# Kernel tuning notes

Hardware: AMD Instinct MI355X
Metric: run time of the kernel (lower is better)

The kernel has to match this reference:

```python
import jax, jax.numpy as jnp
import numpy as np

H, KV, D, S = 32, 8, 128, 2048
HID = H * D
L = S  # cache length
LAYER_IDX = 0


def rotate_half(x, axis):
    x1, x2 = jnp.split(x, 2, axis=axis)
    return jnp.concatenate([-x2, x1], axis=axis)


def setup_inputs() -> dict:
    key = jax.random.key(0)
    ks = jax.random.split(key, 9)
    scale = 0.02
    hidden_states = jax.random.normal(ks[0], (1, HID, 1, S), jnp.float32)
    wq = jax.random.normal(ks[1], (H * D, HID), jnp.float32) * scale
    wk = jax.random.normal(ks[2], (KV * D, HID), jnp.float32) * scale
    wv = jax.random.normal(ks[3], (KV * D, HID), jnp.float32) * scale
    wo = jax.random.normal(ks[4], (HID, H * D), jnp.float32) * scale
    bq = jax.random.normal(ks[5], (H * D,), jnp.float32) * scale
    bk = jax.random.normal(ks[6], (KV * D,), jnp.float32) * scale
    bv = jax.random.normal(ks[7], (KV * D,), jnp.float32) * scale
    # RoPE tables (rotate-half convention): (1,1,S,D) and transposed (1,1,D,S)
    inv_freq = 1.0 / (10000.0 ** (np.arange(0, D, 2, dtype=np.float32) / D))
    t = np.arange(S, dtype=np.float32)
    freqs = np.outer(t, inv_freq)                    # (S, D/2)
    emb = np.concatenate([freqs, freqs], axis=-1)    # (S, D)
    cos = jnp.asarray(np.cos(emb), jnp.float32)[None, None]
    sin = jnp.asarray(np.sin(emb), jnp.float32)[None, None]
    cos_t = jnp.swapaxes(cos, -1, -2)
    sin_t = jnp.swapaxes(sin, -1, -2)
    # causal mask in transposed (cache_len, q_len) layout: key pos l visible iff l <= s
    lpos = np.arange(L)[:, None]
    spos = np.arange(S)[None, :]
    attention_mask = jnp.asarray(np.where(lpos <= spos, 0.0, -1e9).astype(np.float32))[None, None]
    key_cache = jnp.zeros((1, KV, L, D), jnp.float32)
    value_cache = jnp.zeros((1, KV, L, D), jnp.float32)
    return dict(hidden_states=hidden_states, wq=wq, bq=bq, wk=wk, bk=bk, wv=wv, bv=bv,
                wo=wo, cos=cos, sin=sin, cos_t=cos_t, sin_t=sin_t,
                attention_mask=attention_mask, key_cache=key_cache,
                value_cache=value_cache, cache_position=0)


def reference(hidden_states, wq, bq, wk, bk, wv, bv, wo, cos, sin, cos_t, sin_t,
              attention_mask, key_cache, value_cache, cache_position):
    x = hidden_states[0, :, 0, :]                          # (HID, S) channels-first
    q = wq @ x + bq[:, None]                               # (H*D, S)
    k = wk @ x + bk[:, None]                               # (KV*D, S)
    v = wv @ x + bv[:, None]
    q = q.reshape(H, D, S)                                 # (H, D, S)
    k = jnp.swapaxes(k.reshape(KV, D, S), 1, 2)            # (KV, S, D)
    v = jnp.swapaxes(v.reshape(KV, D, S), 1, 2)            # (KV, S, D)
    # RoPE: Q rotated along D (dim=-2 in NCHW), K along last dim
    q = q * cos_t[0] + rotate_half(q, axis=1) * sin_t[0]
    k = k * cos[0] + rotate_half(k, axis=2) * sin[0]
    # KV-cache in-place update at cache_position
    kc = jax.lax.dynamic_update_slice(key_cache, k[None], (LAYER_IDX, 0, cache_position, 0))
    vc = jax.lax.dynamic_update_slice(value_cache, v[None], (LAYER_IDX, 0, cache_position, 0))
    kk = kc[LAYER_IDX]                                     # (KV, L, D)
    vv = vc[LAYER_IDX]                                     # (KV, L, D)
    G = H // KV
    qg = q.reshape(KV, G, D, S)                            # group queries per KV head
    scores = jnp.einsum('kld,kgds->kgls', kk, qg) / jnp.sqrt(jnp.float32(D))
    scores = scores + attention_mask[0]                    # (1,L,S) broadcasts over (KV,G,L,S)
    w = jax.nn.softmax(scores, axis=2)                     # softmax over cache_len
    out = jnp.einsum('kgls,kld->kgsd', w, vv)              # (KV, G, S, D)
    out = jnp.swapaxes(out.reshape(H, S, D), 1, 2).reshape(H * D, S)
    y = wo @ out                                           # (HID, S)
    return y[None, :, None, :]                             # (1, HID, 1, S)
```

## Files before the change

### kernel.cpp

```cpp
#include <hip/hip_runtime.h>
#include <hip/hip_bf16.h>

#define H_   32
#define KV_  8
#define D_   128
#define S_   2048
#define HID_ 4096

typedef __attribute__((ext_vector_type(8))) short short8;
typedef short8 short8a __attribute__((may_alias));
typedef __attribute__((ext_vector_type(4))) float f32x4;
typedef unsigned short u16;
typedef unsigned int u32;

__device__ __forceinline__ u16 f2bf(float f) {
  union { float f; unsigned u; } a; a.f = f;
  unsigned r = a.u + 0x7fffu + ((a.u >> 16) & 1u);
  return (u16)(r >> 16);
}
__device__ __forceinline__ float bf2f(u16 h) {
  union { unsigned u; float f; } a; a.u = ((unsigned)h) << 16;
  return a.f;
}

#define GLOAD16(g, l) __builtin_amdgcn_global_load_lds( \
    (const __attribute__((address_space(1))) void*)(g), \
    (__attribute__((address_space(3))) void*)(l), 16, 0, 0)

__global__ void cast4_kernel(const float* __restrict__ s0, const float* __restrict__ s1,
                             const float* __restrict__ s2, const float* __restrict__ s3,
                             u16* __restrict__ d0, u16* __restrict__ d1,
                             u16* __restrict__ d2, u16* __restrict__ d3,
                             int n0, int n1, int n2, int n3) {
  int total = n0 + n1 + n2 + n3;
  for (int i = blockIdx.x * blockDim.x + threadIdx.x; i < total; i += gridDim.x * blockDim.x) {
    const float* s; u16* d; int k = i;
    if (k < n0) { s = s0; d = d0; }
    else if ((k -= n0) < n1) { s = s1; d = d1; }
    else if ((k -= n1) < n2) { s = s2; d = d2; }
    else { k -= n2; s = s3; d = d3; }
    float4 v = ((const float4*)s)[k];
    ushort4 o;
    o.x = f2bf(v.x); o.y = f2bf(v.y); o.z = f2bf(v.z); o.w = f2bf(v.w);
    ((ushort4*)d)[k] = o;
  }
}

__global__ __launch_bounds__(256) void transpose_cast_kernel(const float* __restrict__ in,
                                                             u16* __restrict__ out) {
  __shared__ float t[32][33];
  int tx = threadIdx.x & 31, ty = threadIdx.x >> 5;
  int s0 = blockIdx.x * 32, c0 = blockIdx.y * 32;
  #pragma unroll
  for (int i = 0; i < 4; i++)
    t[ty + i * 8][tx] = in[(size_t)(c0 + ty + i * 8) * S_ + s0 + tx];
  __syncthreads();
  #pragma unroll
  for (int i = 0; i < 4; i++)
    out[(size_t)(s0 + ty + i * 8) * HID_ + c0 + tx] = f2bf(t[tx][ty + i * 8]);
}

__device__ __forceinline__ short8 ldsfrag(const u16* base, int row, int ks, int kg) {
  int cb = (ks * 64 + kg * 16) ^ ((row & 7) << 4);
  return *(const short8a*)((const char*)base + row * 128 + cb);
}

template<int BM>
__global__ __launch_bounds__(512, 2) void gemm_t(const u16* __restrict__ A, const u16* __restrict__ Bt,
    const float* __restrict__ bq, const float* __restrict__ bk, const float* __restrict__ bv,
    u16* __restrict__ Cb, float* __restrict__ Cf, int N, int K) {
  constexpr int CA = BM / 64;
  constexpr int MI = BM / 64;
  __shared__ alignas(16) u16 Asl[2][BM * 64];
  __shared__ alignas(16) u16 Bsl[2][256 * 64];
  int tid = threadIdx.x, wid = tid >> 6, lane = tid & 63;
  int lr = lane & 15, kg = lane >> 4;
  int gx = gridDim.x, nwg = gx * gridDim.y;
  int lid = blockIdx.y * gx + blockIdx.x;
  int q = nwg >> 3, r = nwg & 7;
  int xcd = lid & 7, idx = lid >> 3;
  int swz = (xcd < r ? xcd * (q + 1) : r * (q + 1) + (xcd - r) * q) + idx;
  int m0 = (swz / gx) * BM, n0 = (swz % gx) * 256;
  const u16* Ap = A + (size_t)m0 * K;
  const u16* Bp = Bt + (size_t)n0 * K;
  int wm = wid >> 2, wn = wid & 3;
  f32x4 acc[2][2][MI][2] = {};
  int NT = K >> 6;

  auto STAGEC = [&](const u16* gp, int tile, int chunk, u16* base) {
    int p = tid * 16;
    int row = (chunk << 6) + (p >> 7);
    int gcb = (p & 127) ^ ((row & 7) << 4);
    const char* src = (const char*)gp + ((size_t)row * K + (tile << 6)) * 2 + gcb;
    char* dst = (char*)base + (chunk << 13) + (wid << 10);
    GLOAD16(src, dst);
  };
  auto LDA = [&](short8 (&af)[MI][2], const u16* base, int qm) {
    #pragma unroll
    for (int mi = 0; mi < MI; mi++)
      #pragma unroll
      for (int ks = 0; ks < 2; ks++)
        af[mi][ks] = ldsfrag(base, wm * (BM / 2) + qm * (BM / 4) + mi * 16 + lr, ks, kg);
  };
  auto LDB = [&](short8 (&bf)[2][2], const u16* base, int qn) {
    #pragma unroll
    for (int ni = 0; ni < 2; ni++)
      #pragma unroll
      for (int ks = 0; ks < 2; ks++)
        bf[ni][ks] = ldsfrag(base, wn * 64 + qn * 32 + ni * 16 + lr, ks, kg);
  };
  auto MM = [&](f32x4 (&a)[MI][2], short8 (&af)[MI][2], short8 (&bf)[2][2]) {
    #pragma unroll
    for (int ks = 0; ks < 2; ks++)
      #pragma unroll
      for (int mi = 0; mi < MI; mi++)
        #pragma unroll
        for (int ni = 0; ni < 2; ni++)
          a[mi][ni] = __builtin_amdgcn_mfma_f32_16x16x32_bf16(af[mi][ks], bf[ni][ks], a[mi][ni], 0, 0, 0);
  };
  #define BAR() __builtin_amdgcn_s_barrier()
  #define SB()  __builtin_amdgcn_sched_barrier(0)
  #define VMCNT(n) asm volatile("s_waitcnt vmcnt(" #n ")" ::: "memory")

  #pragma unroll
  for (int c = 0; c < CA; c++) STAGEC(Ap, 0, c, &Asl[0][0]);
  #pragma unroll
  for (int c = 0; c < 4; c++) STAGEC(Bp, 0, c, &Bsl[0][0]);
  #pragma unroll
  for (int c = 0; c < 4; c++) STAGEC(Bp, 1, c, &Bsl[1][0]);
  VMCNT(4);
  BAR();

  short8 af0[MI][2], af1[MI][2], bfA[2][2], bfB[2][2];
  for (int T = 0; T < NT; T++) {
    int par = T & 1;
    u16* aC = &Asl[par][0];
    u16* bC = &Bsl[par][0];
    u16* aN = &Asl[par ^ 1][0];
    int tA = T + 1 < NT ? T + 1 : NT - 1;
    int tB = T + 2 < NT ? T + 2 : NT - 1;
    LDA(af0, aC, 0); LDA(af1, aC, 1); LDB(bfA, bC, 0); LDB(bfB, bC, 1);
    #pragma unroll
    for (int c = 0; c < CA; c++) STAGEC(Ap, tA, c, aN);
    SB(); BAR();
    __builtin_amdgcn_s_setprio(1);
    MM(acc[0][0], af0, bfA); MM(acc[0][1], af0, bfB);
    __builtin_amdgcn_s_setprio(0);
    BAR();
    STAGEC(Bp, tB, 0, bC); STAGEC(Bp, tB, 1, bC);
    STAGEC(Bp, tB, 2, bC); STAGEC(Bp, tB, 3, bC);
    VMCNT(4);
    SB(); BAR();
    __builtin_amdgcn_s_setprio(1);
    MM(acc[1][0], af1, bfA); MM(acc[1][1], af1, bfB);
    __builtin_amdgcn_s_setprio(0);
    BAR();
  }
  #undef BAR
  #undef SB
  #undef VMCNT

  #pragma unroll
  for (int qm = 0; qm < 2; qm++)
    #pragma unroll
    for (int qn = 0; qn < 2; qn++)
      #pragma unroll
      for (int mi = 0; mi < MI; mi++)
        #pragma unroll
        for (int ni = 0; ni < 2; ni++) {
          int col = n0 + wn * 64 + qn * 32 + ni * 16 + lr;
          int rbase = m0 + wm * (BM / 2) + qm * (BM / 4) + mi * 16 + kg * 4;
          #pragma unroll
          for (int rr = 0; rr < 4; rr++) {
            int row = rbase + rr;
            float v = acc[qm][qn][mi][ni][rr];
            if (bq) v += row < 4096 ? bq[row] : (row < 5120 ? bk[row - 4096] : bv[row - 5120]);
            if (Cf) Cf[(size_t)row * N + col] = v;
            else    Cb[(size_t)row * N + col] = f2bf(v);
          }
        }
}

__global__ __launch_bounds__(256, 2) void gemm128(const u16* __restrict__ A, const u16* __restrict__ Bt,
                                                  float* __restrict__ Cf, int N, int K) {
  __shared__ alignas(16) u16 Asl[2][128 * 64];
  __shared__ alignas(16) u16 Bsl[2][128 * 64];
  int tid = threadIdx.x, wid = tid >> 6, lane = tid & 63;
  int lr = lane & 15, kg = lane >> 4;
  int gx = gridDim.x, nwg = gx * gridDim.y;
  int lid = blockIdx.y * gx + blockIdx.x;
  int q = nwg >> 3, r = nwg & 7;
  int xcd = lid & 7, idx = lid >> 3;
  int swz = (xcd < r ? xcd * (q + 1) : r * (q + 1) + (xcd - r) * q) + idx;
  int m0 = (swz / gx) * 128, n0 = (swz % gx) * 128;
  const u16* Ap = A + (size_t)m0 * K;
  const u16* Bp = Bt + (size_t)n0 * K;
  int wr = wid >> 1, wc = wid & 1;
  f32x4 acc[2][2][2][2] = {};
  int NT = K >> 6;

  auto STAGEC = [&](const u16* gp, int tile, int chunk, u16* base) {
    int p = (chunk << 12) + tid * 16;
    int row = p >> 7;
    int gcb = (p & 127) ^ ((row & 7) << 4);
    const char* src = (const char*)gp + ((size_t)row * K + (tile << 6)) * 2 + gcb;
    char* dst = (char*)base + (chunk << 12) + (wid << 10);
    GLOAD16(src, dst);
  };
  auto LDA = [&](short8 (&af)[2][2], const u16* base, int qm) {
    #pragma unroll
    for (int mi = 0; mi < 2; mi++)
      #pragma unroll
      for (int ks = 0; ks < 2; ks++)
        af[mi][ks] = ldsfrag(base, wr * 64 + qm * 32 + mi * 16 + lr, ks, kg);
  };
  auto LDB = [&](short8 (&bf)[2][2], const u16* base, int qn) {
    #pragma unroll
    for (int ni = 0; ni < 2; ni++)
      #pragma unroll
      for (int ks = 0; ks < 2; ks++)
        bf[ni][ks] = ldsfrag(base, wc * 64 + qn * 32 + ni * 16 + lr, ks, kg);
  };
  auto MM = [&](f32x4 (&a)[2][2], short8 (&af)[2][2], short8 (&bf)[2][2]) {
    #pragma unroll
    for (int ks = 0; ks < 2; ks++)
      #pragma unroll
      for (int mi = 0; mi < 2; mi++)
        #pragma unroll
        for (int ni = 0; ni < 2; ni++)
          a[mi][ni] = __builtin_amdgcn_mfma_f32_16x16x32_bf16(af[mi][ks], bf[ni][ks], a[mi][ni], 0, 0, 0);
  };
  #define BAR() __builtin_amdgcn_s_barrier()
  #define SB()  __builtin_amdgcn_sched_barrier(0)
  #define VMCNT(n) asm volatile("s_waitcnt vmcnt(" #n ")" ::: "memory")

  #pragma unroll
  for (int c = 0; c < 4; c++) STAGEC(Ap, 0, c, &Asl[0][0]);
  #pragma unroll
  for (int c = 0; c < 4; c++) STAGEC(Bp, 0, c, &Bsl[0][0]);
  #pragma unroll
  for (int c = 0; c < 4; c++) STAGEC(Bp, 1, c, &Bsl[1][0]);
  VMCNT(4);
  BAR();

  short8 af0[2][2], af1[2][2], bfA[2][2], bfB[2][2];
  for (int T = 0; T < NT; T++) {
    int par = T & 1;
    u16* aC = &Asl[par][0];
    u16* bC = &Bsl[par][0];
    u16* aN = &Asl[par ^ 1][0];
    int tA = T + 1 < NT ? T + 1 : NT - 1;
    int tB = T + 2 < NT ? T + 2 : NT - 1;
    LDA(af0, aC, 0); LDA(af1, aC, 1); LDB(bfA, bC, 0); LDB(bfB, bC, 1);
    STAGEC(Ap, tA, 0, aN); STAGEC(Ap, tA, 1, aN);
    STAGEC(Ap, tA, 2, aN); STAGEC(Ap, tA, 3, aN);
    SB(); BAR();
    __builtin_amdgcn_s_setprio(1);
    MM(acc[0][0], af0, bfA); MM(acc[0][1], af0, bfB);
    __builtin_amdgcn_s_setprio(0);
    BAR();
    STAGEC(Bp, tB, 0, bC); STAGEC(Bp, tB, 1, bC);
    STAGEC(Bp, tB, 2, bC); STAGEC(Bp, tB, 3, bC);
    VMCNT(4);
    SB(); BAR();
    __builtin_amdgcn_s_setprio(1);
    MM(acc[1][0], af1, bfA); MM(acc[1][1], af1, bfB);
    __builtin_amdgcn_s_setprio(0);
    BAR();
  }
  #undef BAR
  #undef SB
  #undef VMCNT

  #pragma unroll
  for (int qm = 0; qm < 2; qm++)
    #pragma unroll
    for (int qn = 0; qn < 2; qn++)
      #pragma unroll
      for (int mi = 0; mi < 2; mi++)
        #pragma unroll
        for (int ni = 0; ni < 2; ni++) {
          int col = n0 + wc * 64 + qn * 32 + ni * 16 + lr;
          int rbase = m0 + wr * 64 + qm * 32 + mi * 16 + kg * 4;
          #pragma unroll
          for (int rr = 0; rr < 4; rr++)
            Cf[(size_t)(rbase + rr) * N + col] = acc[qm][qn][mi][ni][rr];
        }
}

__global__ __launch_bounds__(256) void rope2_kernel(const u16* __restrict__ qin,
                                                    const u16* __restrict__ kin,
                                                    u16* __restrict__ qout,
                                                    u16* __restrict__ kout,
                                                    const float* __restrict__ cp,
                                                    const float* __restrict__ sp) {
  __shared__ u16 t[128][33];
  int hh = blockIdx.x;
  bool isQ = hh < H_;
  int h = isQ ? hh : hh - H_;
  const u16* in = (isQ ? qin : kin) + (size_t)h * 128 * S_;
  u16* out = (isQ ? qout : kout) + (size_t)h * S_ * D_;
  float oscale = isQ ? 0.1275176329533421f : 1.0f;
  int s0 = blockIdx.y * 32;
  int tid = threadIdx.x;
  #pragma unroll
  for (int i = 0; i < 16; i++) {
    int idx = tid + i * 256;
    int row = idx >> 5, sc = idx & 31;
    t[row][sc] = in[(size_t)row * S_ + s0 + sc];
  }
  __syncthreads();
  int d = tid & 127, sh = tid >> 7;
  int dl = d & 63;
  bool hi = d >= 64;
  #pragma unroll
  for (int j = 0; j < 16; j++) {
    int sl = sh * 16 + j;
    int s = s0 + sl;
    float x = bf2f(t[d][sl]);
    float p = bf2f(t[d ^ 64][sl]);
    float c  = cp[(size_t)s * D_ + dl];
    float sn = sp[(size_t)s * D_ + dl];
    float o = hi ? fmaf(p, sn, x * c) : fmaf(-p, sn, x * c);
    out[(size_t)s * D_ + d] = f2bf(o * oscale);
  }
}

__global__ __launch_bounds__(256) void attn_v2(const u16* __restrict__ Q, const u16* __restrict__ K,
                                               const u16* __restrict__ V, u16* __restrict__ Ot) {
  __shared__ alignas(16) u16 Ks[2][64 * 128];
  __shared__ alignas(16) u16 Vs[2][128 * 64];
  __shared__ alignas(16) u16 Pl[4][2][16 * 64];
  int h = blockIdx.x;
  int qtile = (int)(gridDim.y - 1) - (int)blockIdx.y;
  int kv = h >> 2;
  int tid = threadIdx.x, wid = tid >> 6, lane = tid & 63;
  int lr = lane & 15, kg = lane >> 4;
  int q0w = qtile * 128 + wid * 32;
  const u16* Qb = Q + ((size_t)h * S_ + q0w) * D_;
  const u16* Kb = K + (size_t)kv * S_ * D_;
  const u16* Vb = V + (size_t)kv * D_ * S_;
  int sw = (lr & 7) << 3;

  short8 qf[2][4];
  #pragma unroll
  for (int m = 0; m < 2; m++)
    #pragma unroll
    for (int kk = 0; kk < 4; kk++)
      qf[m][kk] = *(const short8a*)(Qb + (size_t)(m * 16 + lr) * D_ + kk * 32 + kg * 8);

  f32x4 acc[2][8] = {};
  float mreg[2] = {-1e30f, -1e30f};
  float lsum[2] = {0.f, 0.f};

  int krow[4], kcb[4], vrow[4], vcb[4];
  #pragma unroll
  for (int j = 0; j < 4; j++) {
    int c = wid * 4 + j;
    int o = c * 1024 + lane * 16;
    krow[j] = o >> 8;
    kcb[j] = (o & 255) ^ ((krow[j] & 7) << 4);
    vrow[j] = o >> 7;
    vcb[j] = (o & 127) ^ ((vrow[j] & 7) << 4);
  }

  int nlt = 2 * qtile + 2;
  #pragma unroll
  for (int j = 0; j < 4; j++) {
    int c = wid * 4 + j;
    GLOAD16((const char*)Kb + ((size_t)krow[j] * D_) * 2 + kcb[j], (char*)Ks[0] + c * 1024);
    GLOAD16((const char*)Vb + ((size_t)vrow[j] * S_) * 2 + vcb[j], (char*)Vs[0] + c * 1024);
  }
  int cur = 0;
  for (int t = 0; t < nlt; t++) {
    __syncthreads();
    if (t + 1 < nlt) {
      int l1 = (t + 1) * 64;
      #pragma unroll
      for (int j = 0; j < 4; j++) {
        int c = wid * 4 + j;
        GLOAD16((const char*)Kb + ((size_t)(l1 + krow[j]) * D_) * 2 + kcb[j],
                (char*)Ks[cur ^ 1] + c * 1024);
        GLOAD16((const char*)Vb + ((size_t)vrow[j] * S_ + l1) * 2 + vcb[j],
                (char*)Vs[cur ^ 1] + c * 1024);
      }
    }
    int l0 = t * 64;
    bool act0 = l0 <= q0w + 15;
    bool act1 = l0 <= q0w + 31;
    if (act1) {
      const u16* Kc = Ks[cur];
      const u16* Vc = Vs[cur];
      f32x4 st[2][4] = {};
      #pragma unroll
      for (int ls = 0; ls < 4; ls++) {
        short8 kf[4];
        #pragma unroll
        for (int kk = 0; kk < 4; kk++)
          kf[kk] = *(const short8a*)&Kc[(ls * 16 + lr) * 128 + ((kk * 32 + kg * 8) ^ sw)];
        #pragma unroll
        for (int kk = 0; kk < 4; kk++) {
          st[0][ls] = __builtin_amdgcn_mfma_f32_16x16x32_bf16(kf[kk], qf[0][kk], st[0][ls], 0, 0, 0);
          st[1][ls] = __builtin_amdgcn_mfma_f32_16x16x32_bf16(kf[kk], qf[1][kk], st[1][ls], 0, 0, 0);
        }
      }
      #pragma unroll
      for (int m = 0; m < 2; m++) {
        bool act = m ? act1 : act0;
        if (!act) continue;
        int qrow = q0w + m * 16 + lr;
        if (l0 + 63 > q0w + m * 16) {
          #pragma unroll
          for (int ls = 0; ls < 4; ls++)
            #pragma unroll
            for (int rr = 0; rr < 4; rr++) {
              int l = l0 + ls * 16 + kg * 4 + rr;
              st[m][ls][rr] = (l <= qrow) ? st[m][ls][rr] : -1e30f;
            }
        }
        float rmax;
        {
          float a0 = fmaxf(fmaxf(st[m][0][0], st[m][0][1]), fmaxf(st[m][0][2], st[m][0][3]));
          float a1 = fmaxf(fmaxf(st[m][1][0], st[m][1][1]), fmaxf(st[m][1][2], st[m][1][3]));
          float a2 = fmaxf(fmaxf(st[m][2][0], st[m][2][1]), fmaxf(st[m][2][2], st[m][2][3]));
          float a3 = fmaxf(fmaxf(st[m][3][0], st[m][3][1]), fmaxf(st[m][3][2], st[m][3][3]));
          rmax = fmaxf(fmaxf(a0, a1), fmaxf(a2, a3));
        }
        rmax = fmaxf(rmax, __shfl_xor(rmax, 16, 64));
        rmax = fmaxf(rmax, __shfl_xor(rmax, 32, 64));
        if (__any(rmax > mreg[m] + 8.0f)) {
          float nm = fmaxf(mreg[m], rmax);
          float f = __builtin_amdgcn_exp2f(mreg[m] - nm);
          mreg[m] = nm;
          lsum[m] *= f;
          float fr0 = __shfl(f, kg * 4 + 0, 64);
          float fr1 = __shfl(f, kg * 4 + 1, 64);
          float fr2 = __shfl(f, kg * 4 + 2, 64);
          float fr3 = __shfl(f, kg * 4 + 3, 64);
          #pragma unroll
          for (int dc = 0; dc < 8; dc++) {
            acc[m][dc][0] *= fr0; acc[m][dc][1] *= fr1;
            acc[m][dc][2] *= fr2; acc[m][dc][3] *= fr3;
          }
        }
        float e[4][4];
        #pragma unroll
        for (int ls = 0; ls < 4; ls++)
          #pragma unroll
          for (int rr = 0; rr < 4; rr++)
            e[ls][rr] = __builtin_amdgcn_exp2f(st[m][ls][rr] - mreg[m]);
        float rs = 0.f;
        #pragma unroll
        for (int ls = 0; ls < 4; ls++)
          rs += (e[ls][0] + e[ls][1]) + (e[ls][2] + e[ls][3]);
        rs += __shfl_xor(rs, 16, 64);
        rs += __shfl_xor(rs, 32, 64);
        lsum[m] += rs;
        u16* Pw = &Pl[wid][m][0];
        #pragma unroll
        for (int ls = 0; ls < 4; ls++) {
          __hip_bfloat162 p01 = __float22bfloat162_rn(float2{e[ls][0], e[ls][1]});
          __hip_bfloat162 p23 = __float22bfloat162_rn(float2{e[ls][2], e[ls][3]});
          uint2 pk;
          pk.x = *(u32*)&p01;
          pk.y = *(u32*)&p23;
          *(uint2*)&Pw[lr * 64 + ((ls * 16 + kg * 4) ^ sw)] = pk;
        }
      }
      #pragma unroll
      for (int kk = 0; kk < 2; kk++) {
        short8 pf0 = {}, pf1;
        if (act0) pf0 = *(const short8a*)&Pl[wid][0][lr * 64 + ((kk * 32 + kg * 8) ^ sw)];
        pf1 = *(const short8a*)&Pl[wid][1][lr * 64 + ((kk * 32 + kg * 8) ^ sw)];
        #pragma unroll
        for (int dc = 0; dc < 8; dc++) {
          short8 vf = *(const short8a*)&Vc[(dc * 16 + lr) * 64 + ((kk * 32 + kg * 8) ^ sw)];
          if (act0) acc[0][dc] = __builtin_amdgcn_mfma_f32_16x16x32_bf16(pf0, vf, acc[0][dc], 0, 0, 0);
          acc[1][dc] = __builtin_amdgcn_mfma_f32_16x16x32_bf16(pf1, vf, acc[1][dc], 0, 0, 0);
        }
      }
    }
    cur ^= 1;
  }
  #pragma unroll
  for (int m = 0; m < 2; m++) {
    float inv0 = 1.0f / __shfl(lsum[m], kg * 4 + 0, 64);
    float inv1 = 1.0f / __shfl(lsum[m], kg * 4 + 1, 64);
    float inv2 = 1.0f / __shfl(lsum[m], kg * 4 + 2, 64);
    float inv3 = 1.0f / __shfl(lsum[m], kg * 4 + 3, 64);
    #pragma unroll
    for (int dc = 0; dc < 8; dc++) {
      int col = h * D_ + dc * 16 + lr;
      int qg = q0w + m * 16 + kg * 4;
      Ot[(size_t)(qg + 0) * HID_ + col] = f2bf(acc[m][dc][0] * inv0);
      Ot[(size_t)(qg + 1) * HID_ + col] = f2bf(acc[m][dc][1] * inv1);
      Ot[(size_t)(qg + 2) * HID_ + col] = f2bf(acc[m][dc][2] * inv2);
      Ot[(size_t)(qg + 3) * HID_ + col] = f2bf(acc[m][dc][3] * inv3);
    }
  }
}

static constexpr size_t OFF_WQKV = 0;
static constexpr size_t OFF_WO   = 50331648;
static constexpr size_t OFF_XT   = 83886080;
static constexpr size_t OFF_QKVC = 100663296;

extern "C" void kernel_launch(void* const* d_in, const int* in_sizes, int n_in,
                              void* d_out, int out_size, void* d_ws, size_t ws_size,
                              hipStream_t stream) {
  const float* x    = (const float*)d_in[0];
  const float* wq   = (const float*)d_in[1];
  const float* bq   = (const float*)d_in[2];
  const float* wk   = (const float*)d_in[3];
  const float* bk   = (const float*)d_in[4];
  const float* wv   = (const float*)d_in[5];
  const float* bv   = (const float*)d_in[6];
  const float* wo   = (const float*)d_in[7];
  const float* cosP = (const float*)d_in[8];
  const float* sinP = (const float*)d_in[9];
  char* ws = (char*)d_ws;
  u16* WQKV = (u16*)(ws + OFF_WQKV);
  u16* WO   = (u16*)(ws + OFF_WO);
  u16* XT   = (u16*)(ws + OFF_XT);
  u16* QKVC = (u16*)(ws + OFF_QKVC);
  u16* QT   = QKVC;
  u16* KT   = QKVC + (size_t)4096 * S_;
  u16* VB   = QKVC + (size_t)5120 * S_;
  u16* QATT = (u16*)(ws + 0);
  u16* KATT = (u16*)(ws + 16777216);
  u16* OT   = (u16*)(ws + 20971520);
  float* y = (float*)d_out;

  cast4_kernel<<<2048, 256, 0, stream>>>(
      wq, wk, wv, wo,
      WQKV, WQKV + (size_t)4096 * HID_, WQKV + (size_t)5120 * HID_, WO,
      (HID_ * HID_) / 4, (KV_ * D_ * HID_) / 4, (KV_ * D_ * HID_) / 4, (HID_ * HID_) / 4);
  transpose_cast_kernel<<<dim3(S_ / 32, HID_ / 32), 256, 0, stream>>>(x, XT);
  gemm_t<192><<<dim3(S_ / 256, 6144 / 192), 512, 0, stream>>>(WQKV, XT, bq, bk, bv,
                                                              QKVC, nullptr, S_, HID_);
  rope2_kernel<<<dim3(H_ + KV_, S_ / 32), 256, 0, stream>>>(QT, KT, QATT, KATT, cosP, sinP);
  attn_v2<<<dim3(H_, S_ / 128), 256, 0, stream>>>(QATT, KATT, VB, OT);
  gemm128<<<dim3(S_ / 128, HID_ / 128), 256, 0, stream>>>(WO, OT, y, S_, HID_);
}
```

Baseline: 334.2 us.

## Triple-buffer B tiles and merge GEMM main loop into one barrier phase

Both GEMM kernels now keep three LDS buffers for the B operand instead of two, rotating separate read and write indices. Each iteration issues the global-to-LDS staging for the next A tile and the B tile two steps ahead up front. It then waits on a vmcnt threshold, does one barrier, loads all fragments and runs both MFMA halves back to back. This removes the mid-iteration barrier pair and the separate B staging phase, at the cost of extra LDS, which may limit occupancy. It also depends on vmcnt counts matching the number of loads per iteration, which is fragile for the BM-templated kernel.

```diff
diff --git a/kernel.cpp b/kernel.cpp
--- a/kernel.cpp
+++ b/kernel.cpp
@@ -72,7 +72,7 @@
   constexpr int CA = BM / 64;
   constexpr int MI = BM / 64;
   __shared__ alignas(16) u16 Asl[2][BM * 64];
-  __shared__ alignas(16) u16 Bsl[2][256 * 64];
+  __shared__ alignas(16) u16 Bsl[3][256 * 64];
   int tid = threadIdx.x, wid = tid >> 6, lane = tid & 63;
   int lr = lane & 15, kg = lane >> 4;
   int gx = gridDim.x, nwg = gx * gridDim.y;
@@ -128,33 +128,31 @@
   for (int c = 0; c < 4; c++) STAGEC(Bp, 0, c, &Bsl[0][0]);
   #pragma unroll
   for (int c = 0; c < 4; c++) STAGEC(Bp, 1, c, &Bsl[1][0]);
-  VMCNT(4);
-  BAR();
 
   short8 af0[MI][2], af1[MI][2], bfA[2][2], bfB[2][2];
+  int rb = 0, wb = 2;
   for (int T = 0; T < NT; T++) {
     int par = T & 1;
-    u16* aC = &Asl[par][0];
-    u16* bC = &Bsl[par][0];
+    const u16* aC = &Asl[par][0];
     u16* aN = &Asl[par ^ 1][0];
+    const u16* bR = &Bsl[rb][0];
+    u16* bW = &Bsl[wb][0];
     int tA = T + 1 < NT ? T + 1 : NT - 1;
     int tB = T + 2 < NT ? T + 2 : NT - 1;
-    LDA(af0, aC, 0); LDA(af1, aC, 1); LDB(bfA, bC, 0); LDB(bfB, bC, 1);
     #pragma unroll
     for (int c = 0; c < CA; c++) STAGEC(Ap, tA, c, aN);
-    SB(); BAR();
+    #pragma unroll
+    for (int c = 0; c < 4; c++) STAGEC(Bp, tB, c, bW);
+    VMCNT(7);
+    SB(); BAR(); SB();
+    LDA(af0, aC, 0); LDA(af1, aC, 1); LDB(bfA, bR, 0); LDB(bfB, bR, 1);
     __builtin_amdgcn_s_setprio(1);
     MM(acc[0][0], af0, bfA); MM(acc[0][1], af0, bfB);
-    __builtin_amdgcn_s_setprio(0);
-    BAR();
-    STAGEC(Bp, tB, 0, bC); STAGEC(Bp, tB, 1, bC);
-    STAGEC(Bp, tB, 2, bC); STAGEC(Bp, tB, 3, bC);
-    VMCNT(4);
-    SB(); BAR();
-    __builtin_amdgcn_s_setprio(1);
     MM(acc[1][0], af1, bfA); MM(acc[1][1], af1, bfB);
     __builtin_amdgcn_s_setprio(0);
     BAR();
+    rb = rb == 2 ? 0 : rb + 1;
+    wb = wb == 2 ? 0 : wb + 1;
   }
   #undef BAR
   #undef SB
@@ -184,7 +182,7 @@
 __global__ __launch_bounds__(256, 2) void gemm128(const u16* __restrict__ A, const u16* __restrict__ Bt,
                                                   float* __restrict__ Cf, int N, int K) {
   __shared__ alignas(16) u16 Asl[2][128 * 64];
-  __shared__ alignas(16) u16 Bsl[2][128 * 64];
+  __shared__ alignas(16) u16 Bsl[3][128 * 64];
   int tid = threadIdx.x, wid = tid >> 6, lane = tid & 63;
   int lr = lane & 15, kg = lane >> 4;
   int gx = gridDim.x, nwg = gx * gridDim.y;
@@ -240,33 +238,31 @@
   for (int c = 0; c < 4; c++) STAGEC(Bp, 0, c, &Bsl[0][0]);
   #pragma unroll
   for (int c = 0; c < 4; c++) STAGEC(Bp, 1, c, &Bsl[1][0]);
-  VMCNT(4);
-  BAR();
 
   short8 af0[2][2], af1[2][2], bfA[2][2], bfB[2][2];
+  int rb = 0, wb = 2;
   for (int T = 0; T < NT; T++) {
     int par = T & 1;
-    u16* aC = &Asl[par][0];
-    u16* bC = &Bsl[par][0];
+    const u16* aC = &Asl[par][0];
     u16* aN = &Asl[par ^ 1][0];
+    const u16* bR = &Bsl[rb][0];
+    u16* bW = &Bsl[wb][0];
     int tA = T + 1 < NT ? T + 1 : NT - 1;
     int tB = T + 2 < NT ? T + 2 : NT - 1;
-    LDA(af0, aC, 0); LDA(af1, aC, 1); LDB(bfA, bC, 0); LDB(bfB, bC, 1);
-    STAGEC(Ap, tA, 0, aN); STAGEC(Ap, tA, 1, aN);
-    STAGEC(Ap, tA, 2, aN); STAGEC(Ap, tA, 3, aN);
-    SB(); BAR();
+    #pragma unroll
+    for (int c = 0; c < 4; c++) STAGEC(Ap, tA, c, aN);
+    #pragma unroll
+    for (int c = 0; c < 4; c++) STAGEC(Bp, tB, c, bW);
+    VMCNT(8);
+    SB(); BAR(); SB();
+    LDA(af0, aC, 0); LDA(af1, aC, 1); LDB(bfA, bR, 0); LDB(bfB, bR, 1);
     __builtin_amdgcn_s_setprio(1);
     MM(acc[0][0], af0, bfA); MM(acc[0][1], af0, bfB);
-    __builtin_amdgcn_s_setprio(0);
-    BAR();
-    STAGEC(Bp, tB, 0, bC); STAGEC(Bp, tB, 1, bC);
-    STAGEC(Bp, tB, 2, bC); STAGEC(Bp, tB, 3, bC);
-    VMCNT(4);
-    SB(); BAR();
-    __builtin_amdgcn_s_setprio(1);
     MM(acc[1][0], af1, bfA); MM(acc[1][1], af1, bfB);
     __builtin_amdgcn_s_setprio(0);
     BAR();
+    rb = rb == 2 ? 0 : rb + 1;
+    wb = wb == 2 ? 0 : wb + 1;
   }
   #undef BAR
   #undef SB
```

After: 349.9 us. 4.7% more time.
